# Kernel tuning notes

Measured on AMD Instinct MI355X. Metric: run time of the kernel, lower is better.

## Reference

```python
import jax, jax.numpy as jnp
import numpy as np
from jax import lax

# pywt db4 filters (8 taps)
_DEC_LO = np.array([-0.010597401784997278, 0.032883011666982945, 0.030841381835986965,
                    -0.18703481171888114, -0.02798376941698385, 0.6308807679295904,
                    0.7148465705525415, 0.23037781330885523])
_DEC_HI = np.array([-0.23037781330885523, 0.7148465705525415, -0.6308807679295904,
                    -0.02798376941698385, 0.18703481171888114, 0.030841381835986965,
                    -0.032883011666982945, -0.010597401784997278])
_REC_LO = _DEC_LO[::-1].copy()
_REC_HI = _DEC_HI[::-1].copy()
_L = 8  # filter length
LEVELS = 4


def _dwt_level(x):
    # x: (M, n) -> (cA, cD) each (M, (n+_L-1)//2), pywt 'symmetric' mode
    xe = jnp.pad(x, ((0, 0), (_L - 1, _L - 1)), mode='symmetric')[:, 1:]
    ker = jnp.stack([_DEC_LO[::-1], _DEC_HI[::-1]]).astype(x.dtype)[:, None, :]  # (2,1,L)
    y = lax.conv_general_dilated(xe[:, None, :], ker, (2,), 'VALID')  # (M,2,m)
    return y[:, 0], y[:, 1]


def _idwt_level(ca, cd, out_len):
    # inverse DWT, cropped to out_len (matches length of next-finer approximation)
    inp = jnp.stack([ca, cd], axis=1)  # (M,2,m)
    ker = jnp.stack([_REC_LO[::-1], _REC_HI[::-1]]).astype(ca.dtype)[None]  # (1,2,L)
    y = lax.conv_general_dilated(inp, ker, (1,), [(_L - 1, _L - 1)], lhs_dilation=(2,))
    return y[:, 0, _L - 2:_L - 2 + out_len]


def setup_inputs() -> dict:
    key = jax.random.key(0)
    k1, k2, k3, k4 = jax.random.split(key, 4)
    B, N, C = 32, 8192, 64
    m = N
    for _ in range(LEVELS):
        m = (m + _L - 1) // 2  # 518
    scale = 1.0 / (C * C)
    return {
        'x': jax.random.normal(k1, (B, N, C), jnp.float32),
        'w1': scale * jax.random.uniform(k2, (C, C, m), jnp.float32),
        'w2': scale * jax.random.uniform(k3, (C, C, m), jnp.float32),
        'dense_kernel': jax.random.normal(k4, (C, C), jnp.float32) / jnp.sqrt(C).astype(jnp.float32),
        'dense_bias': jnp.zeros((C,), jnp.float32),
    }


def reference(x, w1, w2, dense_kernel, dense_bias):
    B, N, C = x.shape
    xc = jnp.transpose(x, (0, 2, 1)).reshape(B * C, N)  # per-(batch,channel) signals
    # analysis: multi-level DWT
    lens, details = [], []
    a = xc
    for _ in range(LEVELS):
        lens.append(a.shape[1])
        a, d = _dwt_level(a)
        details.append(d)
    m = a.shape[1]
    # channel mixing on coarsest approximation and coarsest detail (WNO kernel)
    a = jnp.einsum('bim,iom->bom', a.reshape(B, C, m), w1).reshape(B * C, m)
    details[-1] = jnp.einsum('bim,iom->bom', details[-1].reshape(B, C, m), w2).reshape(B * C, m)
    # synthesis: multi-level IDWT
    for j in range(LEVELS - 1, -1, -1):
        a = _idwt_level(a, details[j], lens[j])
    y = jnp.transpose(a.reshape(B, C, N), (0, 2, 1))
    shortcut = x @ dense_kernel + dense_bias  # Dense 1x1 shortcut
    out = y + shortcut
    return out * jnp.tanh(jax.nn.softplus(out))  # mish
```

## Files before the change

kernel.cpp:

```cpp
#include <hip/hip_runtime.h>
#include <hip/hip_bf16.h>
#include <stdint.h>

typedef __attribute__((ext_vector_type(8))) short short8;
typedef __attribute__((ext_vector_type(4))) float floatx4;

__device__ __constant__ float c_DL[8] = {
    -0.010597401784997278f, 0.032883011666982945f, 0.030841381835986965f,
    -0.18703481171888114f, -0.02798376941698385f, 0.6308807679295904f,
    0.7148465705525415f, 0.23037781330885523f};
__device__ __constant__ float c_DH[8] = {
    -0.23037781330885523f, 0.7148465705525415f, -0.6308807679295904f,
    -0.02798376941698385f, 0.18703481171888114f, 0.030841381835986965f,
    -0.032883011666982945f, -0.010597401784997278f};
__device__ __constant__ float c_RL[8] = {
    0.23037781330885523f, 0.7148465705525415f, 0.6308807679295904f,
    -0.02798376941698385f, -0.18703481171888114f, 0.030841381835986965f,
    0.032883011666982945f, -0.010597401784997278f};
__device__ __constant__ float c_RH[8] = {
    -0.010597401784997278f, -0.032883011666982945f, 0.030841381835986965f,
    0.18703481171888114f, -0.02798376941698385f, -0.6308807679295904f,
    0.7148465705525415f, -0.23037781330885523f};

__device__ __forceinline__ float bflo(uint32_t u) { return __uint_as_float(u << 16); }
__device__ __forceinline__ float bfhi(uint32_t u) { return __uint_as_float(u & 0xffff0000u); }
__device__ __forceinline__ float ldf(const float* p, size_t i) { return p[i]; }
__device__ __forceinline__ float ldf(const __hip_bfloat16* p, size_t i) { return __bfloat162float(p[i]); }
__device__ __forceinline__ void stf(float* p, size_t i, float v) { p[i] = v; }
__device__ __forceinline__ void stf(__hip_bfloat16* p, size_t i, float v) { p[i] = __float2bfloat16(v); }
__device__ __forceinline__ short f2bs(float f) {
  __hip_bfloat16 h = __float2bfloat16(f);
  return *reinterpret_cast<short*>(&h);
}

__device__ __forceinline__ int reflect_idx(int t, int n) {
  if (t < 0) t = -1 - t;
  if (t >= n) t = 2 * n - 1 - t;
  return t;
}

#define S1R 4100
#define S2R 2056

__global__ __launch_bounds__(256) void k_wT(const float* __restrict__ w1,
                                            const float* __restrict__ w2,
                                            float* __restrict__ wt1,
                                            float* __restrict__ wt2) {
  const float* w = blockIdx.z ? w2 : w1;
  float* wt = blockIdx.z ? wt2 : wt1;
  const int io0 = blockIdx.x * 64;
  const int p0 = blockIdx.y * 64;
  const int pw = min(64, 518 - p0);
  const int tid = threadIdx.x;
  __shared__ float ts[64 * 65];
  for (int idx = tid; idx < 64 * 64; idx += 256) {
    int row = idx >> 6, col = idx & 63;
    if (col < pw) ts[row * 65 + col] = w[(size_t)(io0 + row) * 518 + p0 + col];
  }
  __syncthreads();
  for (int idx = tid; idx < 64 * 64; idx += 256) {
    int pl = idx >> 6, io = idx & 63;
    if (pl < pw) wt[(size_t)(p0 + pl) * 4096 + io0 + io] = ts[io * 65 + pl];
  }
}

#define NT1 134
__global__ __launch_bounds__(256) void k_dwt_first(const float* __restrict__ x,
                                                   __hip_bfloat16* __restrict__ outa,
                                                   __hip_bfloat16* __restrict__ outd) {
  const int b = blockIdx.y;
  const int k0 = blockIdx.x * 64;
  const int tid = threadIdx.x;
  __shared__ float xs[NT1 * 65];

  const float4* x4 = (const float4*)x;
  for (int idx = tid; idx < NT1 * 16; idx += 256) {
    int nl = idx >> 4, cq = idx & 15;
    int t = 2 * k0 - 6 + nl;
    int n = reflect_idx(t, 8192);
    float4 v = x4[((size_t)b * 8192 + n) * 16 + cq];
    float* d = &xs[nl * 65 + 4 * cq];
    d[0] = v.x; d[1] = v.y; d[2] = v.z; d[3] = v.w;
  }
  __syncthreads();

  const int kk = tid & 63;
  const int k = k0 + kk;
  if (k >= 4099) return;
  for (int c = (tid >> 6); c < 64; c += 4) {
    float lo = 0.f, hi = 0.f;
#pragma unroll
    for (int j = 0; j < 8; ++j) {
      float v = xs[(2 * kk + 7 - j) * 65 + c];
      lo += c_DL[j] * v;
      hi += c_DH[j] * v;
    }
    size_t s = (size_t)b * 64 + c;
    outa[s * S1R + k] = __float2bfloat16(lo);
    outd[s * S1R + k] = __float2bfloat16(hi);
  }
}

__global__ __launch_bounds__(256) void k_ana234(const __hip_bfloat16* __restrict__ a1,
                                                __hip_bfloat16* __restrict__ d2o,
                                                float* __restrict__ d3o,
                                                float* __restrict__ a4o,
                                                float* __restrict__ d4o) {
  const int bid = blockIdx.x;
  const int s = (bid & 7) * 256 + (bid >> 3);
  const int i_ch = s >> 5;
  const int bb = s & 31;
  const int r = bb * 64 + i_ch;
  const int tid = threadIdx.x;
  __shared__ float s1[4100];
  __shared__ float s2[2054];
  __shared__ float s3[1032];

  const uint2* row2 = (const uint2*)(a1 + (size_t)r * S1R);
  for (int i = tid; i < 1025; i += 256) {
    uint2 u = row2[i];
    int e = 4 * i;
    s1[e] = bflo(u.x); s1[e + 1] = bfhi(u.x);
    s1[e + 2] = bflo(u.y); s1[e + 3] = bfhi(u.y);
  }
  __syncthreads();

  for (int k = tid; k < 2053; k += 256) {
    float lo = 0.f, hi = 0.f;
    if (k >= 3 && k <= 2048) {
      const float2* p = (const float2*)&s1[2 * k - 6];
      float2 v0 = p[0], v1 = p[1], v2 = p[2], v3 = p[3];
      lo = c_RL[0]*v0.x + c_RL[1]*v0.y + c_RL[2]*v1.x + c_RL[3]*v1.y +
           c_RL[4]*v2.x + c_RL[5]*v2.y + c_RL[6]*v3.x + c_RL[7]*v3.y;
      hi = c_RH[0]*v0.x + c_RH[1]*v0.y + c_RH[2]*v1.x + c_RH[3]*v1.y +
           c_RH[4]*v2.x + c_RH[5]*v2.y + c_RH[6]*v3.x + c_RH[7]*v3.y;
    } else {
#pragma unroll
      for (int j = 0; j < 8; ++j) {
        float v = s1[reflect_idx(2 * k + 1 - j, 4099)];
        lo += c_DL[j] * v; hi += c_DH[j] * v;
      }
    }
    d2o[(size_t)r * S2R + k] = __float2bfloat16(hi);
    s2[k] = lo;
  }
  __syncthreads();

  for (int k = tid; k < 1030; k += 256) {
    float lo = 0.f, hi = 0.f;
    if (k >= 3 && k <= 1025) {
      const float2* p = (const float2*)&s2[2 * k - 6];
      float2 v0 = p[0], v1 = p[1], v2 = p[2], v3 = p[3];
      lo = c_RL[0]*v0.x + c_RL[1]*v0.y + c_RL[2]*v1.x + c_RL[3]*v1.y +
           c_RL[4]*v2.x + c_RL[5]*v2.y + c_RL[6]*v3.x + c_RL[7]*v3.y;
      hi = c_RH[0]*v0.x + c_RH[1]*v0.y + c_RH[2]*v1.x + c_RH[3]*v1.y +
           c_RH[4]*v2.x + c_RH[5]*v2.y + c_RH[6]*v3.x + c_RH[7]*v3.y;
    } else {
#pragma unroll
      for (int j = 0; j < 8; ++j) {
        float v = s2[reflect_idx(2 * k + 1 - j, 2053)];
        lo += c_DL[j] * v; hi += c_DH[j] * v;
      }
    }
    d3o[(size_t)r * 1030 + k] = hi;
    s3[k] = lo;
  }
  __syncthreads();

  for (int k = tid; k < 518; k += 256) {
    float lo = 0.f, hi = 0.f;
    if (k >= 3 && k <= 514) {
      const float2* p = (const float2*)&s3[2 * k - 6];
      float2 v0 = p[0], v1 = p[1], v2 = p[2], v3 = p[3];
      lo = c_RL[0]*v0.x + c_RL[1]*v0.y + c_RL[2]*v1.x + c_RL[3]*v1.y +
           c_RL[4]*v2.x + c_RL[5]*v2.y + c_RL[6]*v3.x + c_RL[7]*v3.y;
      hi = c_RH[0]*v0.x + c_RH[1]*v0.y + c_RH[2]*v1.x + c_RH[3]*v1.y +
           c_RH[4]*v2.x + c_RH[5]*v2.y + c_RH[6]*v3.x + c_RH[7]*v3.y;
    } else {
#pragma unroll
      for (int j = 0; j < 8; ++j) {
        float v = s3[reflect_idx(2 * k + 1 - j, 1030)];
        lo += c_DL[j] * v; hi += c_DH[j] * v;
      }
    }
    a4o[(size_t)k * 2048 + s] = lo;
    d4o[(size_t)k * 2048 + s] = hi;
  }
}

__global__ __launch_bounds__(256) void k_mix_pc(const float* __restrict__ wt1,
                                                const float* __restrict__ wt2,
                                                const float* __restrict__ a4t,
                                                const float* __restrict__ d4t,
                                                float* __restrict__ am,
                                                float* __restrict__ dm) {
  const int bx = blockIdx.x;
  const int xcd = bx & 7;
  const int j = bx >> 3;
  const int p = (xcd < 6) ? (xcd * 65 + j) : (390 + (xcd - 6) * 64 + j);

  const float* w = blockIdx.y ? wt2 : wt1;
  const float* act = blockIdx.y ? d4t : a4t;
  float* outp = blockIdx.y ? dm : am;

  __shared__ float ws[4096];
  __shared__ float as_[2048];
  const int tid = threadIdx.x;

  const float4* wg = (const float4*)(w + (size_t)p * 4096);
  const float4* ag = (const float4*)(act + (size_t)p * 2048);
  float4* ws4 = (float4*)ws;
  float4* as4 = (float4*)as_;
  for (int t = tid; t < 1024; t += 256) ws4[t] = wg[t];
  for (int t = tid; t < 512; t += 256) as4[t] = ag[t];
  __syncthreads();

  const int o0 = (tid & 15) * 4;
  const int bq = tid >> 4;
  floatx4 acc0 = {0.f, 0.f, 0.f, 0.f}, acc1 = {0.f, 0.f, 0.f, 0.f};

#pragma unroll 8
  for (int i = 0; i < 64; ++i) {
    floatx4 wv = *(const floatx4*)&ws[i * 64 + o0];
    float a0 = as_[i * 32 + bq];
    float a1 = as_[i * 32 + bq + 16];
#pragma unroll
    for (int q = 0; q < 4; ++q) {
      acc0[q] += a0 * wv[q];
      acc1[q] += a1 * wv[q];
    }
  }

#pragma unroll
  for (int q = 0; q < 4; ++q) {
    outp[(size_t)(bq * 64 + o0 + q) * 518 + p] = acc0[q];
    outp[(size_t)((bq + 16) * 64 + o0 + q) * 518 + p] = acc1[q];
  }
}

__global__ __launch_bounds__(256) void k_syn32(const float* __restrict__ a4m,
                                               const float* __restrict__ d4m,
                                               const float* __restrict__ d3,
                                               __hip_bfloat16* __restrict__ r2out) {
  const int r = blockIdx.x;
  const int tid = threadIdx.x;
  __shared__ float sa[518], sd[518], s3d[1030], r3[1030];
  for (int i = tid; i < 518; i += 256) {
    sa[i] = a4m[(size_t)r * 518 + i];
    sd[i] = d4m[(size_t)r * 518 + i];
  }
  for (int i = tid; i < 1030; i += 256) s3d[i] = d3[(size_t)r * 1030 + i];
  __syncthreads();
  for (int s = tid; s < 1030; s += 256) {
    int u = s >> 1, par = s & 1;
    float acc = 0.f;
#pragma unroll
    for (int t = 0; t < 4; ++t) {
      int i = u + 3 - t;
      float fl = par ? c_RL[2 * t + 1] : c_RL[2 * t];
      float fh = par ? c_RH[2 * t + 1] : c_RH[2 * t];
      acc += fl * sa[i] + fh * sd[i];
    }
    r3[s] = acc;
  }
  __syncthreads();
  for (int s = tid; s < 2053; s += 256) {
    int u = s >> 1, par = s & 1;
    float acc = 0.f;
#pragma unroll
    for (int t = 0; t < 4; ++t) {
      int i = u + 3 - t;
      float fl = par ? c_RL[2 * t + 1] : c_RL[2 * t];
      float fh = par ? c_RH[2 * t + 1] : c_RH[2 * t];
      acc += fl * r3[i] + fh * s3d[i];
    }
    r2out[(size_t)r * S2R + s] = __float2bfloat16(acc);
  }
}

template <typename TCa, typename TCd, typename TOut>
__global__ void k_idwt(const TCa* __restrict__ ca, const TCd* __restrict__ cd,
                       TOut* __restrict__ out, int m, int out_len, int sin, int sout) {
  int s = blockIdx.x * blockDim.x + threadIdx.x;
  if (s >= out_len) return;
  const TCa* pa = ca + (size_t)blockIdx.y * sin;
  const TCd* pd = cd + (size_t)blockIdx.y * sin;
  int u = s >> 1, par = s & 1;
  float acc = 0.f;
#pragma unroll
  for (int t = 0; t < 4; ++t) {
    int i = u + 3 - t;
    float fl = par ? c_RL[2 * t + 1] : c_RL[2 * t];
    float fh = par ? c_RH[2 * t + 1] : c_RH[2 * t];
    acc += fl * ldf(pa, i) + fh * ldf(pd, i);
  }
  stf(out, (size_t)blockIdx.y * sout + s, acc);
}

__global__ __launch_bounds__(256) void k_epilogue(const __hip_bfloat16* __restrict__ r1,
                                                  const __hip_bfloat16* __restrict__ dd1,
                                                  const float* __restrict__ x,
                                                  const float* __restrict__ dk,
                                                  const float* __restrict__ bias,
                                                  float* __restrict__ out) {
  const int b = blockIdx.y;
  const int n0 = blockIdx.x * 64;
  const int u0 = n0 >> 1;
  const int tid = threadIdx.x;
  const int lane = tid & 63;
  const int w = tid >> 6;

  __shared__ __hip_bfloat16 Kt[64 * 72];
  __shared__ float ra[35 * 65];
  __shared__ float rd[35 * 65];

  {
    const float4* dk4 = (const float4*)dk;
    for (int idx = tid; idx < 1024; idx += 256) {
      int c = idx >> 4, o0 = (idx & 15) * 4;
      float4 v = dk4[idx];
      Kt[(o0 + 0) * 72 + c] = __float2bfloat16(v.x);
      Kt[(o0 + 1) * 72 + c] = __float2bfloat16(v.y);
      Kt[(o0 + 2) * 72 + c] = __float2bfloat16(v.z);
      Kt[(o0 + 3) * 72 + c] = __float2bfloat16(v.w);
    }
  }
  {
    int o2 = tid >> 2;
    const __hip_bfloat16* pr = r1 + (size_t)(b * 64 + o2) * S1R + u0;
    const __hip_bfloat16* pd = dd1 + (size_t)(b * 64 + o2) * S1R + u0;
    for (int il = (tid & 3); il < 35; il += 4) {
      ra[il * 65 + o2] = __bfloat162float(pr[il]);
      rd[il * 65 + o2] = __bfloat162float(pd[il]);
    }
  }
  __syncthreads();

  const int m16 = lane & 15;
  const int kq = (lane >> 4) * 8;
  const int nrow = w * 16 + m16;
  const float* xrow = x + ((size_t)b * 8192 + n0 + nrow) * 64;

  floatx4 acc[4];
#pragma unroll
  for (int ot = 0; ot < 4; ++ot) acc[ot] = (floatx4){0.f, 0.f, 0.f, 0.f};

#pragma unroll
  for (int ks = 0; ks < 2; ++ks) {
    float4 xa = *(const float4*)(xrow + ks * 32 + kq);
    float4 xb = *(const float4*)(xrow + ks * 32 + kq + 4);
    short8 af;
    af[0] = f2bs(xa.x); af[1] = f2bs(xa.y); af[2] = f2bs(xa.z); af[3] = f2bs(xa.w);
    af[4] = f2bs(xb.x); af[5] = f2bs(xb.y); af[6] = f2bs(xb.z); af[7] = f2bs(xb.w);
#pragma unroll
    for (int ot = 0; ot < 4; ++ot) {
      short8 bf = *(const short8*)&Kt[(ot * 16 + m16) * 72 + ks * 32 + kq];
      acc[ot] = __builtin_amdgcn_mfma_f32_16x16x32_bf16(af, bf, acc[ot], 0, 0, 0);
    }
  }

  const int rbase = (lane >> 4) * 4;
#pragma unroll
  for (int ot = 0; ot < 4; ++ot) {
    int o_loc = ot * 16 + m16;
    float bo = bias[o_loc];
#pragma unroll
    for (int rg = 0; rg < 4; ++rg) {
      int n_loc = w * 16 + rbase + rg;
      int ul = n_loc >> 1, par = n_loc & 1;
      float wv = 0.f;
#pragma unroll
      for (int t = 0; t < 4; ++t) {
        int i = ul + 3 - t;
        float fl = par ? c_RL[2 * t + 1] : c_RL[2 * t];
        float fh = par ? c_RH[2 * t + 1] : c_RH[2 * t];
        wv += fl * ra[i * 65 + o_loc] + fh * rd[i * 65 + o_loc];
      }
      float v = acc[ot][rg] + wv + bo;
      float e = __expf(fminf(v, 15.f));
      float num = e * (e + 2.f);
      float mm = (v > 15.f) ? v : v * (num / (num + 2.f));
      out[((size_t)b * 8192 + n0 + n_loc) * 64 + o_loc] = mm;
    }
  }
}

extern "C" void kernel_launch(void* const* d_in, const int* in_sizes, int n_in,
                              void* d_out, int out_size, void* d_ws, size_t ws_size,
                              hipStream_t stream) {
  const float* x    = (const float*)d_in[0];
  const float* w1   = (const float*)d_in[1];
  const float* w2   = (const float*)d_in[2];
  const float* dk   = (const float*)d_in[3];
  const float* bias = (const float*)d_in[4];
  float* out = (float*)d_out;

  const size_t R = 2048;

  float* wf = (float*)d_ws;
  float* d3f = wf; wf += R * 1030;
  float* a4t = wf; wf += R * 518;
  float* d4t = wf; wf += R * 518;
  float* a4m = wf; wf += R * 518;
  float* d4m = wf; wf += R * 518;
  float* wt1 = wf; wf += (size_t)518 * 4096;
  float* wt2 = wf; wf += (size_t)518 * 4096;
  __hip_bfloat16* wb = (__hip_bfloat16*)wf;
  __hip_bfloat16* a1b = wb; wb += R * S1R;
  __hip_bfloat16* d1b = wb; wb += R * S1R;
  __hip_bfloat16* a2b = wb; wb += R * S2R;
  __hip_bfloat16* d2b = wb; wb += R * S2R;

  k_wT<<<dim3(64, 9, 2), 256, 0, stream>>>(w1, w2, wt1, wt2);
  k_dwt_first<<<dim3(65, 32), 256, 0, stream>>>(x, a1b, d1b);
  k_ana234<<<dim3(2048), 256, 0, stream>>>(a1b, d2b, d3f, a4t, d4t);
  k_mix_pc<<<dim3(518, 2), 256, 0, stream>>>(wt1, wt2, a4t, d4t, a4m, d4m);
  k_syn32<<<dim3(2048), 256, 0, stream>>>(a4m, d4m, d3f, a2b);
  k_idwt<__hip_bfloat16, __hip_bfloat16, __hip_bfloat16>
      <<<dim3((4099 + 255) / 256, 2048), 256, 0, stream>>>(a2b, d2b, a1b, 2053, 4099, S2R, S1R);
  k_epilogue<<<dim3(128, 32), 256, 0, stream>>>(a1b, d1b, x, dk, bias, out);
}
```

Measured before the change: 285.1 us.

## Fuse level-2 IDWT into synthesis kernel; vectorize epilogue loads, nontemporal stores

Merges the separate level-2 inverse DWT kernel into the shared-memory synthesis kernel, so each row runs levels 4→3→2→1 on-chip and the bf16 level-2 approximation never round-trips through global memory. The epilogue now loads its bf16 reconstruction tiles as ushort4 vectors into a padded shared layout, and writes its output with nontemporal stores. This saves one kernel launch and one intermediate buffer. The cost is more shared memory per block in the synthesis kernel, which may lower occupancy.

```diff
diff --git a/kernel.cpp b/kernel.cpp
--- a/kernel.cpp
+++ b/kernel.cpp
@@ -24,10 +24,7 @@
 
 __device__ __forceinline__ float bflo(uint32_t u) { return __uint_as_float(u << 16); }
 __device__ __forceinline__ float bfhi(uint32_t u) { return __uint_as_float(u & 0xffff0000u); }
-__device__ __forceinline__ float ldf(const float* p, size_t i) { return p[i]; }
-__device__ __forceinline__ float ldf(const __hip_bfloat16* p, size_t i) { return __bfloat162float(p[i]); }
-__device__ __forceinline__ void stf(float* p, size_t i, float v) { p[i] = v; }
-__device__ __forceinline__ void stf(__hip_bfloat16* p, size_t i, float v) { p[i] = __float2bfloat16(v); }
+__device__ __forceinline__ float bfu(unsigned short u) { return __uint_as_float(((uint32_t)u) << 16); }
 __device__ __forceinline__ short f2bs(float f) {
   __hip_bfloat16 h = __float2bfloat16(f);
   return *reinterpret_cast<short*>(&h);
@@ -238,18 +235,28 @@
   }
 }
 
-__global__ __launch_bounds__(256) void k_syn32(const float* __restrict__ a4m,
-                                               const float* __restrict__ d4m,
-                                               const float* __restrict__ d3,
-                                               __hip_bfloat16* __restrict__ r2out) {
+__global__ __launch_bounds__(256) void k_syn(const float* __restrict__ a4m,
+                                             const float* __restrict__ d4m,
+                                             const float* __restrict__ d3,
+                                             const __hip_bfloat16* __restrict__ d2,
+                                             __hip_bfloat16* __restrict__ r1out) {
   const int r = blockIdx.x;
   const int tid = threadIdx.x;
-  __shared__ float sa[518], sd[518], s3d[1030], r3[1030];
+  __shared__ float sa[518], sd[518], s3d[1030], r3[1030], d2s[2056], r2[2053];
   for (int i = tid; i < 518; i += 256) {
     sa[i] = a4m[(size_t)r * 518 + i];
     sd[i] = d4m[(size_t)r * 518 + i];
   }
   for (int i = tid; i < 1030; i += 256) s3d[i] = d3[(size_t)r * 1030 + i];
+  {
+    const uint2* p2 = (const uint2*)(d2 + (size_t)r * S2R);
+    for (int i = tid; i < 514; i += 256) {
+      uint2 u = p2[i];
+      int e = 4 * i;
+      d2s[e] = bflo(u.x); d2s[e + 1] = bfhi(u.x);
+      d2s[e + 2] = bflo(u.y); d2s[e + 3] = bfhi(u.y);
+    }
+  }
   __syncthreads();
   for (int s = tid; s < 1030; s += 256) {
     int u = s >> 1, par = s & 1;
@@ -274,29 +281,24 @@
       float fh = par ? c_RH[2 * t + 1] : c_RH[2 * t];
       acc += fl * r3[i] + fh * s3d[i];
     }
-    r2out[(size_t)r * S2R + s] = __float2bfloat16(acc);
-  }
-}
-
-template <typename TCa, typename TCd, typename TOut>
-__global__ void k_idwt(const TCa* __restrict__ ca, const TCd* __restrict__ cd,
-                       TOut* __restrict__ out, int m, int out_len, int sin, int sout) {
-  int s = blockIdx.x * blockDim.x + threadIdx.x;
-  if (s >= out_len) return;
-  const TCa* pa = ca + (size_t)blockIdx.y * sin;
-  const TCd* pd = cd + (size_t)blockIdx.y * sin;
-  int u = s >> 1, par = s & 1;
-  float acc = 0.f;
-#pragma unroll
-  for (int t = 0; t < 4; ++t) {
-    int i = u + 3 - t;
-    float fl = par ? c_RL[2 * t + 1] : c_RL[2 * t];
-    float fh = par ? c_RH[2 * t + 1] : c_RH[2 * t];
-    acc += fl * ldf(pa, i) + fh * ldf(pd, i);
-  }
-  stf(out, (size_t)blockIdx.y * sout + s, acc);
-}
-
+    r2[s] = acc;
+  }
+  __syncthreads();
+  for (int s = tid; s < 4099; s += 256) {
+    int u = s >> 1, par = s & 1;
+    float acc = 0.f;
+#pragma unroll
+    for (int t = 0; t < 4; ++t) {
+      int i = u + 3 - t;
+      float fl = par ? c_RL[2 * t + 1] : c_RL[2 * t];
+      float fh = par ? c_RH[2 * t + 1] : c_RH[2 * t];
+      acc += fl * r2[i] + fh * d2s[i];
+    }
+    r1out[(size_t)r * S1R + s] = __float2bfloat16(acc);
+  }
+}
+
+#define RAS 68
 __global__ __launch_bounds__(256) void k_epilogue(const __hip_bfloat16* __restrict__ r1,
                                                   const __hip_bfloat16* __restrict__ dd1,
                                                   const float* __restrict__ x,
@@ -311,8 +313,8 @@
   const int w = tid >> 6;
 
   __shared__ __hip_bfloat16 Kt[64 * 72];
-  __shared__ float ra[35 * 65];
-  __shared__ float rd[35 * 65];
+  __shared__ float ra[36 * RAS];
+  __shared__ float rd[36 * RAS];
 
   {
     const float4* dk4 = (const float4*)dk;
@@ -327,11 +329,20 @@
   }
   {
     int o2 = tid >> 2;
-    const __hip_bfloat16* pr = r1 + (size_t)(b * 64 + o2) * S1R + u0;
-    const __hip_bfloat16* pd = dd1 + (size_t)(b * 64 + o2) * S1R + u0;
-    for (int il = (tid & 3); il < 35; il += 4) {
-      ra[il * 65 + o2] = __bfloat162float(pr[il]);
-      rd[il * 65 + o2] = __bfloat162float(pd[il]);
+    const ushort4* pr4 = (const ushort4*)(r1 + (size_t)(b * 64 + o2) * S1R + u0);
+    const ushort4* pd4 = (const ushort4*)(dd1 + (size_t)(b * 64 + o2) * S1R + u0);
+    for (int q = tid & 3; q < 9; q += 4) {
+      ushort4 v = pr4[q];
+      int i0 = 4 * q;
+      ra[(i0 + 0) * RAS + o2] = bfu(v.x);
+      ra[(i0 + 1) * RAS + o2] = bfu(v.y);
+      ra[(i0 + 2) * RAS + o2] = bfu(v.z);
+      ra[(i0 + 3) * RAS + o2] = bfu(v.w);
+      ushort4 d = pd4[q];
+      rd[(i0 + 0) * RAS + o2] = bfu(d.x);
+      rd[(i0 + 1) * RAS + o2] = bfu(d.y);
+      rd[(i0 + 2) * RAS + o2] = bfu(d.z);
+      rd[(i0 + 3) * RAS + o2] = bfu(d.w);
     }
   }
   __syncthreads();
@@ -374,13 +385,13 @@
         int i = ul + 3 - t;
         float fl = par ? c_RL[2 * t + 1] : c_RL[2 * t];
         float fh = par ? c_RH[2 * t + 1] : c_RH[2 * t];
-        wv += fl * ra[i * 65 + o_loc] + fh * rd[i * 65 + o_loc];
+        wv += fl * ra[i * RAS + o_loc] + fh * rd[i * RAS + o_loc];
       }
       float v = acc[ot][rg] + wv + bo;
       float e = __expf(fminf(v, 15.f));
       float num = e * (e + 2.f);
       float mm = (v > 15.f) ? v : v * (num / (num + 2.f));
-      out[((size_t)b * 8192 + n0 + n_loc) * 64 + o_loc] = mm;
+      __builtin_nontemporal_store(mm, &out[((size_t)b * 8192 + n0 + n_loc) * 64 + o_loc]);
     }
   }
 }
@@ -408,15 +419,12 @@
   __hip_bfloat16* wb = (__hip_bfloat16*)wf;
   __hip_bfloat16* a1b = wb; wb += R * S1R;
   __hip_bfloat16* d1b = wb; wb += R * S1R;
-  __hip_bfloat16* a2b = wb; wb += R * S2R;
   __hip_bfloat16* d2b = wb; wb += R * S2R;
 
   k_wT<<<dim3(64, 9, 2), 256, 0, stream>>>(w1, w2, wt1, wt2);
   k_dwt_first<<<dim3(65, 32), 256, 0, stream>>>(x, a1b, d1b);
   k_ana234<<<dim3(2048), 256, 0, stream>>>(a1b, d2b, d3f, a4t, d4t);
   k_mix_pc<<<dim3(518, 2), 256, 0, stream>>>(wt1, wt2, a4t, d4t, a4m, d4m);
-  k_syn32<<<dim3(2048), 256, 0, stream>>>(a4m, d4m, d3f, a2b);
-  k_idwt<__hip_bfloat16, __hip_bfloat16, __hip_bfloat16>
-      <<<dim3((4099 + 255) / 256, 2048), 256, 0, stream>>>(a2b, d2b, a1b, 2053, 4099, S2R, S1R);
+  k_syn<<<dim3(2048), 256, 0, stream>>>(a4m, d4m, d3f, d2b, a1b);
   k_epilogue<<<dim3(128, 32), 256, 0, stream>>>(a1b, d1b, x, dk, bias, out);
 }
```

Result: faster. 251.9 us (-11.6%).
